# Kernel optimization log

Measured on AMD Instinct MI355X. Metric: run time of the kernel, lower is better.

The kernel has to match this reference:

```python
import jax, jax.numpy as jnp
import numpy as np

BN_EPS = 1e-5

def _bn(h, gamma, beta, mean, var):
    # inference-mode BatchNorm1d
    return (h - mean) * jax.lax.rsqrt(var + BN_EPS) * gamma + beta


def setup_inputs() -> dict:
    key = jax.random.key(0)
    ks = jax.random.split(key, 16)
    N, E, D_in, D, L = 100000, 640000, 256, 128, 3
    s = 0.05
    return {
        "x": jax.random.normal(ks[0], (N, D_in), jnp.float32),
        "edge_index": jax.random.randint(ks[1], (2, E), 0, N, jnp.int32),
        "W_in": jax.random.normal(ks[2], (D_in, D), jnp.float32) * s,
        "b_in": jax.random.normal(ks[3], (D,), jnp.float32) * s,
        "bn_in_gamma": jax.random.uniform(ks[4], (D,), jnp.float32, 0.5, 1.5),
        "bn_in_beta": jax.random.normal(ks[5], (D,), jnp.float32) * s,
        "bn_in_mean": jax.random.normal(ks[6], (D,), jnp.float32) * s,
        "bn_in_var": jax.random.uniform(ks[7], (D,), jnp.float32, 0.5, 1.5),
        "Wl": jax.random.normal(ks[8], (L, D, D), jnp.float32) * s,
        "bl": jax.random.normal(ks[9], (L, D), jnp.float32) * s,
        "Wr": jax.random.normal(ks[10], (L, D, D), jnp.float32) * s,
        "bn_gamma": jax.random.uniform(ks[11], (L, D), jnp.float32, 0.5, 1.5),
        "bn_beta": jax.random.normal(ks[12], (L, D), jnp.float32) * s,
        "bn_mean": jax.random.normal(ks[13], (L, D), jnp.float32) * s,
        "bn_var": jax.random.uniform(ks[14], (L, D), jnp.float32, 0.5, 1.5),
    }


def reference(x, edge_index, W_in, b_in, bn_in_gamma, bn_in_beta, bn_in_mean,
              bn_in_var, Wl, bl, Wr, bn_gamma, bn_beta, bn_mean, bn_var):
    N = x.shape[0]
    src, dst = edge_index[0], edge_index[1]
    # in-degree (clamped to 1 so isolated nodes aggregate to 0, matching PyG mean)
    deg = jax.ops.segment_sum(jnp.ones_like(dst, jnp.float32), dst, num_segments=N)
    deg = jnp.maximum(deg, 1.0)[:, None]  # [N, 1]

    # input projection + BN + ReLU (dropout = identity in eval)
    h = jax.nn.relu(_bn(x @ W_in + b_in, bn_in_gamma, bn_in_beta, bn_in_mean, bn_in_var))

    L = Wl.shape[0]
    for l in range(L):
        # SAGEConv(mean): lin_l(mean_j h_j) + lin_r(h_i)
        agg = jax.ops.segment_sum(h[src], dst, num_segments=N) / deg  # [N, D]
        h_new = agg @ Wl[l] + bl[l] + h @ Wr[l]
        h_new = jax.nn.relu(_bn(h_new, bn_gamma[l], bn_beta[l], bn_mean[l], bn_var[l]))
        h = h + h_new  # residual
    return h
```

## Files before the change

### kernel.cpp

```cpp
#include <hip/hip_runtime.h>

#define BN_EPS 1e-5f

typedef __bf16 bf16x8 __attribute__((ext_vector_type(8)));
typedef float f32x4 __attribute__((ext_vector_type(4)));
typedef unsigned int uint;
typedef unsigned short ushort;

__device__ __forceinline__ ushort f2bf(float f) {
  union { float f; uint u; } v; v.f = f;
  uint r = v.u + 0x7FFF + ((v.u >> 16) & 1);
  return (ushort)(r >> 16);
}
__device__ __forceinline__ float bf2f_lo(uint u) {
  union { uint i; float f; } v; v.i = u << 16; return v.f;
}
__device__ __forceinline__ float bf2f_hi(uint u) {
  union { uint i; float f; } v; v.i = u & 0xffff0000u; return v.f;
}
__device__ __forceinline__ uint pack2(float a, float b) {
  return (uint)f2bf(a) | ((uint)f2bf(b) << 16);
}

__device__ __forceinline__ void lds_barrier() {
  asm volatile("" ::: "memory");
  __builtin_amdgcn_s_waitcnt(0xC07F);
  __builtin_amdgcn_s_barrier();
  asm volatile("" ::: "memory");
}


__global__ void hist_kernel(const int* __restrict__ dst, int* __restrict__ cnt, int E) {
  int e = blockIdx.x * 256 + threadIdx.x;
  if (e < E) atomicAdd(&cnt[dst[e]], 1);
}

__device__ __forceinline__ int block_exscan256(int v, int tid, int* ws4) {
  __syncthreads();
  int lane = tid & 63, w = tid >> 6;
  int x = v;
  #pragma unroll
  for (int off = 1; off < 64; off <<= 1) {
    int y = __shfl_up(x, off, 64);
    if (lane >= off) x += y;
  }
  if (lane == 63) ws4[w] = x;
  __syncthreads();
  if (tid == 0) {
    int s = 0;
    for (int i = 0; i < 4; ++i) { int t = ws4[i]; ws4[i] = s; s += t; }
  }
  __syncthreads();
  return ws4[w] + x - v;
}

__global__ void blocksum_kernel(const int* __restrict__ cnt, int* __restrict__ bsum, int N) {
  __shared__ int ws4[4];
  int tid = threadIdx.x;
  int i = blockIdx.x * 256 + tid;
  int v = (i < N) ? cnt[i] : 0;
  #pragma unroll
  for (int off = 32; off > 0; off >>= 1) v += __shfl_down(v, off, 64);
  if ((tid & 63) == 0) ws4[tid >> 6] = v;
  __syncthreads();
  if (tid == 0) bsum[blockIdx.x] = ws4[0] + ws4[1] + ws4[2] + ws4[3];
}

__global__ void scanbsum_kernel(const int* __restrict__ bsum, int* __restrict__ boff,
                                int NB, int* __restrict__ rowptr, int N, int E) {
  __shared__ int ws4[4];
  __shared__ int tot;
  int tid = threadIdx.x;
  int carry = 0;
  for (int base = 0; base < NB; base += 256) {
    int i = base + tid;
    int v = (i < NB) ? bsum[i] : 0;
    int ex = block_exscan256(v, tid, ws4);
    if (i < NB) boff[i] = carry + ex;
    if (tid == 255) tot = ex + v;
    __syncthreads();
    carry += tot;
  }
  if (tid == 0) rowptr[N] = E;
}

__global__ void writerowptr_kernel(const int* __restrict__ cnt, const int* __restrict__ boff,
                                   int* __restrict__ rowptr, int N) {
  __shared__ int ws4[4];
  int tid = threadIdx.x;
  int i = blockIdx.x * 256 + tid;
  int v = (i < N) ? cnt[i] : 0;
  int ex = block_exscan256(v, tid, ws4);
  if (i < N) rowptr[i] = boff[blockIdx.x] + ex;
}

__global__ void fill_kernel(const int* __restrict__ src, const int* __restrict__ dst,
                            const int* __restrict__ rowptr, int* __restrict__ cur,
                            int* __restrict__ col, int E) {
  int e = blockIdx.x * 256 + threadIdx.x;
  if (e < E) {
    int d = dst[e];
    int p = rowptr[d] + atomicAdd(&cur[d], 1);
    col[p] = src[e];
  }
}

__global__ void deginv_kernel(const int* __restrict__ rowptr, float* __restrict__ dinv, int N) {
  int i = blockIdx.x * 256 + threadIdx.x;
  if (i < N) {
    int d = rowptr[i + 1] - rowptr[i];
    dinv[i] = 1.0f / (float)(d > 0 ? d : 1);
  }
}


__global__ void prep_weights_fm(const float* __restrict__ W_in, const float* __restrict__ Wl,
                                const float* __restrict__ Wr, ushort* __restrict__ Bfm) {
  int p = blockIdx.x * 256 + threadIdx.x;
  int mat = p >> 12;
  int rem = p & 4095;
  int half = rem >> 11;
  int rem2 = rem & 2047;
  int nt = rem2 >> 8, kt2 = (rem2 >> 6) & 3, lane = rem2 & 63;
  int n = nt * 16 + (lane & 15);
  int k0 = (half * 4 + kt2) * 32 + (lane >> 4) * 8;
  ushort tmp[8];
  #pragma unroll
  for (int j = 0; j < 8; ++j) {
    int k = k0 + j;
    float v;
    if (mat == 0) v = W_in[k * 128 + n];
    else {
      int l = mat - 1;
      v = (k < 128) ? Wl[l * 16384 + k * 128 + n] : Wr[l * 16384 + (k - 128) * 128 + n];
    }
    tmp[j] = f2bf(v);
  }
  *(uint4*)&Bfm[(size_t)p * 8] = *(const uint4*)tmp;
}


__global__ void agg_kernel(const int* __restrict__ rowptr, const int* __restrict__ col,
                           const float* __restrict__ dinv, const ushort* __restrict__ h,
                           ushort* __restrict__ agg, int N) {
  int node = blockIdx.x * 8 + (threadIdx.x >> 5);
  if (node >= N) return;
  int lane = threadIdx.x & 31;
  const ushort* hp = h + lane * 4;
  int beg = rowptr[node], end = rowptr[node + 1];
  float a0 = 0.f, a1 = 0.f, a2 = 0.f, a3 = 0.f;
  int e = beg;
  for (; e + 3 < end; e += 4) {
    uint2 v0 = *(const uint2*)(hp + (size_t)col[e] * 128);
    uint2 v1 = *(const uint2*)(hp + (size_t)col[e + 1] * 128);
    uint2 v2 = *(const uint2*)(hp + (size_t)col[e + 2] * 128);
    uint2 v3 = *(const uint2*)(hp + (size_t)col[e + 3] * 128);
    a0 += (bf2f_lo(v0.x) + bf2f_lo(v1.x)) + (bf2f_lo(v2.x) + bf2f_lo(v3.x));
    a1 += (bf2f_hi(v0.x) + bf2f_hi(v1.x)) + (bf2f_hi(v2.x) + bf2f_hi(v3.x));
    a2 += (bf2f_lo(v0.y) + bf2f_lo(v1.y)) + (bf2f_lo(v2.y) + bf2f_lo(v3.y));
    a3 += (bf2f_hi(v0.y) + bf2f_hi(v1.y)) + (bf2f_hi(v2.y) + bf2f_hi(v3.y));
  }
  for (; e < end; ++e) {
    uint2 v0 = *(const uint2*)(hp + (size_t)col[e] * 128);
    a0 += bf2f_lo(v0.x); a1 += bf2f_hi(v0.x);
    a2 += bf2f_lo(v0.y); a3 += bf2f_hi(v0.y);
  }
  float di = dinv[node];
  uint2 o;
  o.x = pack2(a0 * di, a1 * di);
  o.y = pack2(a2 * di, a3 * di);
  *(uint2*)(agg + (size_t)node * 128 + lane * 4) = o;
}


template<bool F32OUT>
__global__ __launch_bounds__(256, 3)
void gemm_layer(const ushort* __restrict__ A0, const ushort* __restrict__ A1,
                const ushort* __restrict__ Bfm, const float* __restrict__ bias,
                const float* __restrict__ gamma, const float* __restrict__ beta,
                const float* __restrict__ mean, const float* __restrict__ var,
                const ushort* __restrict__ residual, void* __restrict__ out, int N) {
  __shared__ ushort Bs[16384];
  int tid = threadIdx.x, wave = tid >> 6, lane = tid & 63;
  int wm = wave >> 1, wn = wave & 1, quad = lane >> 4, l16 = lane & 15;
  int m0 = blockIdx.x * 128;

  int rowm[4];
  #pragma unroll
  for (int mt = 0; mt < 4; ++mt) {
    int r = m0 + wm * 64 + mt * 16 + l16;
    rowm[mt] = r < N ? r : N - 1;
  }

  uint4 a_buf[2][4];
  #pragma unroll
  for (int mt = 0; mt < 4; ++mt)
    a_buf[0][mt] = *(const uint4*)(A0 + (size_t)rowm[mt] * 128 + quad * 8);

  #pragma unroll
  for (int i = 0; i < 8; ++i) {
    int idx = i * 256 + tid;
    *(uint4*)&Bs[idx * 8] = *(const uint4*)&Bfm[idx * 8];
  }
  lds_barrier();

  f32x4 acc[4][4] = {};

  #pragma unroll
  for (int h = 0; h < 2; ++h) {
    #pragma unroll
    for (int k2 = 0; k2 < 4; ++k2) {
      int kt = h * 4 + k2;
      if (kt < 7) {
        const ushort* bse = (kt + 1 < 4) ? A0 : A1;
        int ko = ((kt + 1) & 3) * 32 + quad * 8;
        #pragma unroll
        for (int mt = 0; mt < 4; ++mt)
          a_buf[(kt + 1) & 1][mt] = *(const uint4*)(bse + (size_t)rowm[mt] * 128 + ko);
      }
      bf16x8 bfr[4];
      #pragma unroll
      for (int nt = 0; nt < 4; ++nt)
        bfr[nt] = *(bf16x8*)&Bs[(((wn * 4 + nt) * 4 + k2) * 64 + lane) * 8];
      #pragma unroll
      for (int mt = 0; mt < 4; ++mt) {
        bf16x8 af = __builtin_bit_cast(bf16x8, a_buf[kt & 1][mt]);
        #pragma unroll
        for (int nt = 0; nt < 4; ++nt)
          acc[mt][nt] = __builtin_amdgcn_mfma_f32_16x16x32_bf16(af, bfr[nt], acc[mt][nt], 0, 0, 0);
      }
    }
    if (h == 0) {
      lds_barrier();
      #pragma unroll
      for (int i = 0; i < 8; ++i) {
        int idx = i * 256 + tid;
        *(uint4*)&Bs[idx * 8] = *(const uint4*)&Bfm[16384 + idx * 8];
      }
      lds_barrier();
    }
  }

  #pragma unroll
  for (int nt = 0; nt < 4; ++nt) {
    int c = wn * 64 + nt * 16 + l16;
    float sc = gamma[c] * rsqrtf(var[c] + BN_EPS);
    float sh = beta[c] - mean[c] * sc;
    float bi = bias[c];
    #pragma unroll
    for (int mt = 0; mt < 4; ++mt)
      #pragma unroll
      for (int r = 0; r < 4; ++r)
        acc[mt][nt][r] = fmaxf((acc[mt][nt][r] + bi) * sc + sh, 0.f);
  }

  lds_barrier();
  float* Cb = (float*)Bs + wave * (16 * 68);
  #pragma unroll
  for (int mt = 0; mt < 4; ++mt) {
    #pragma unroll
    for (int nt = 0; nt < 4; ++nt)
      #pragma unroll
      for (int r = 0; r < 4; ++r)
        Cb[(quad * 4 + r) * 68 + nt * 16 + l16] = acc[mt][nt][r];
    #pragma unroll
    for (int i = 0; i < 4; ++i) {
      int idx = i * 64 + lane, rowl = idx >> 4, seg = idx & 15;
      int grow = m0 + wm * 64 + mt * 16 + rowl;
      if (grow < N) {
        float4 vv = *(float4*)&Cb[rowl * 68 + seg * 4];
        uint2 rv = *(const uint2*)(residual + (size_t)grow * 128 + wn * 64 + seg * 4);
        vv.x += bf2f_lo(rv.x); vv.y += bf2f_hi(rv.x);
        vv.z += bf2f_lo(rv.y); vv.w += bf2f_hi(rv.y);
        if (F32OUT) {
          *(float4*)((float*)out + (size_t)grow * 128 + wn * 64 + seg * 4) = vv;
        } else {
          uint2 o;
          o.x = pack2(vv.x, vv.y); o.y = pack2(vv.z, vv.w);
          *(uint2*)((ushort*)out + (size_t)grow * 128 + wn * 64 + seg * 4) = o;
        }
      }
    }
  }
}


__global__ __launch_bounds__(256, 3)
void gemm_in(const float* __restrict__ X, const ushort* __restrict__ Bfm,
             const float* __restrict__ bias,
             const float* __restrict__ gamma, const float* __restrict__ beta,
             const float* __restrict__ mean, const float* __restrict__ var,
             ushort* __restrict__ out, int N) {
  __shared__ ushort Bs[16384];
  int tid = threadIdx.x, wave = tid >> 6, lane = tid & 63;
  int wm = wave >> 1, wn = wave & 1, quad = lane >> 4, l16 = lane & 15;
  int m0 = blockIdx.x * 128;

  int rowm[4];
  #pragma unroll
  for (int mt = 0; mt < 4; ++mt) {
    int r = m0 + wm * 64 + mt * 16 + l16;
    rowm[mt] = r < N ? r : N - 1;
  }

  float4 f_buf[2][4][2];
  #pragma unroll
  for (int mt = 0; mt < 4; ++mt) {
    const float* p = X + (size_t)rowm[mt] * 256 + quad * 8;
    f_buf[0][mt][0] = *(const float4*)p;
    f_buf[0][mt][1] = *(const float4*)(p + 4);
  }

  #pragma unroll
  for (int i = 0; i < 8; ++i) {
    int idx = i * 256 + tid;
    *(uint4*)&Bs[idx * 8] = *(const uint4*)&Bfm[idx * 8];
  }
  lds_barrier();

  f32x4 acc[4][4] = {};

  #pragma unroll
  for (int h = 0; h < 2; ++h) {
    #pragma unroll
    for (int k2 = 0; k2 < 4; ++k2) {
      int kt = h * 4 + k2;
      if (kt < 7) {
        int ko = (kt + 1) * 32 + quad * 8;
        #pragma unroll
        for (int mt = 0; mt < 4; ++mt) {
          const float* p = X + (size_t)rowm[mt] * 256 + ko;
          f_buf[(kt + 1) & 1][mt][0] = *(const float4*)p;
          f_buf[(kt + 1) & 1][mt][1] = *(const float4*)(p + 4);
        }
      }
      bf16x8 bfr[4];
      #pragma unroll
      for (int nt = 0; nt < 4; ++nt)
        bfr[nt] = *(bf16x8*)&Bs[(((wn * 4 + nt) * 4 + k2) * 64 + lane) * 8];
      #pragma unroll
      for (int mt = 0; mt < 4; ++mt) {
        float4 lo = f_buf[kt & 1][mt][0], hi = f_buf[kt & 1][mt][1];
        uint4 av;
        av.x = pack2(lo.x, lo.y); av.y = pack2(lo.z, lo.w);
        av.z = pack2(hi.x, hi.y); av.w = pack2(hi.z, hi.w);
        bf16x8 af = __builtin_bit_cast(bf16x8, av);
        #pragma unroll
        for (int nt = 0; nt < 4; ++nt)
          acc[mt][nt] = __builtin_amdgcn_mfma_f32_16x16x32_bf16(af, bfr[nt], acc[mt][nt], 0, 0, 0);
      }
    }
    if (h == 0) {
      lds_barrier();
      #pragma unroll
      for (int i = 0; i < 8; ++i) {
        int idx = i * 256 + tid;
        *(uint4*)&Bs[idx * 8] = *(const uint4*)&Bfm[16384 + idx * 8];
      }
      lds_barrier();
    }
  }

  #pragma unroll
  for (int nt = 0; nt < 4; ++nt) {
    int c = wn * 64 + nt * 16 + l16;
    float sc = gamma[c] * rsqrtf(var[c] + BN_EPS);
    float sh = beta[c] - mean[c] * sc;
    float bi = bias[c];
    #pragma unroll
    for (int mt = 0; mt < 4; ++mt)
      #pragma unroll
      for (int r = 0; r < 4; ++r)
        acc[mt][nt][r] = fmaxf((acc[mt][nt][r] + bi) * sc + sh, 0.f);
  }

  lds_barrier();
  float* Cb = (float*)Bs + wave * (16 * 68);
  #pragma unroll
  for (int mt = 0; mt < 4; ++mt) {
    #pragma unroll
    for (int nt = 0; nt < 4; ++nt)
      #pragma unroll
      for (int r = 0; r < 4; ++r)
        Cb[(quad * 4 + r) * 68 + nt * 16 + l16] = acc[mt][nt][r];
    #pragma unroll
    for (int i = 0; i < 4; ++i) {
      int idx = i * 64 + lane, rowl = idx >> 4, seg = idx & 15;
      int grow = m0 + wm * 64 + mt * 16 + rowl;
      if (grow < N) {
        float4 vv = *(float4*)&Cb[rowl * 68 + seg * 4];
        uint2 o;
        o.x = pack2(vv.x, vv.y); o.y = pack2(vv.z, vv.w);
        *(uint2*)(out + (size_t)grow * 128 + wn * 64 + seg * 4) = o;
      }
    }
  }
}


extern "C" void kernel_launch(void* const* d_in, const int* in_sizes, int n_in,
                              void* d_out, int out_size, void* d_ws, size_t ws_size,
                              hipStream_t stream) {
  const float* x      = (const float*)d_in[0];
  const int*   eidx   = (const int*)d_in[1];
  const float* W_in   = (const float*)d_in[2];
  const float* b_in   = (const float*)d_in[3];
  const float* bng_in = (const float*)d_in[4];
  const float* bnb_in = (const float*)d_in[5];
  const float* bnm_in = (const float*)d_in[6];
  const float* bnv_in = (const float*)d_in[7];
  const float* Wl     = (const float*)d_in[8];
  const float* bl     = (const float*)d_in[9];
  const float* Wr     = (const float*)d_in[10];
  const float* bng    = (const float*)d_in[11];
  const float* bnb    = (const float*)d_in[12];
  const float* bnm    = (const float*)d_in[13];
  const float* bnv    = (const float*)d_in[14];

  const int N = in_sizes[0] / 256;
  const int E = in_sizes[1] / 2;
  const int NB = (N + 255) / 256;
  const int* src = eidx;
  const int* dst = eidx + E;

  char* ws = (char*)d_ws;
  size_t off = 0;
  auto alloc = [&](size_t bytes) {
    void* p = ws + off;
    off = (off + bytes + 255) & ~(size_t)255;
    return p;
  };
  int* cnt      = (int*)alloc((size_t)N * 4);
  int* rowptr   = (int*)alloc((size_t)(N + 1) * 4);
  int* bsum     = (int*)alloc((size_t)NB * 4);
  int* boff     = (int*)alloc((size_t)NB * 4);
  int* col      = (int*)alloc((size_t)E * 4);
  float* dinv   = (float*)alloc((size_t)N * 4);
  ushort* Bfm   = (ushort*)alloc(4 * 32768 * 2);
  ushort* hA    = (ushort*)alloc((size_t)N * 128 * 2);
  ushort* hB    = (ushort*)alloc((size_t)N * 128 * 2);
  ushort* agg   = (ushort*)alloc((size_t)N * 128 * 2);
  (void)ws_size; (void)n_in; (void)out_size;

  const int EB = (E + 255) / 256;
  const int GB = (N + 127) / 128;

  hipMemsetAsync(cnt, 0, (size_t)N * 4, stream);
  hist_kernel<<<EB, 256, 0, stream>>>(dst, cnt, E);
  blocksum_kernel<<<NB, 256, 0, stream>>>(cnt, bsum, N);
  scanbsum_kernel<<<1, 256, 0, stream>>>(bsum, boff, NB, rowptr, N, E);
  writerowptr_kernel<<<NB, 256, 0, stream>>>(cnt, boff, rowptr, N);
  hipMemsetAsync(cnt, 0, (size_t)N * 4, stream);
  fill_kernel<<<EB, 256, 0, stream>>>(src, dst, rowptr, cnt, col, E);
  deginv_kernel<<<NB, 256, 0, stream>>>(rowptr, dinv, N);

  prep_weights_fm<<<64, 256, 0, stream>>>(W_in, Wl, Wr, Bfm);

  gemm_in<<<GB, 256, 0, stream>>>(x, Bfm, b_in, bng_in, bnb_in, bnm_in, bnv_in, hA, N);

  ushort* hbuf[2] = { hA, hB };
  for (int l = 0; l < 3; ++l) {
    const ushort* h_in = hbuf[l & 1];
    agg_kernel<<<(N + 7) / 8, 256, 0, stream>>>(rowptr, col, dinv, h_in, agg, N);
    const ushort* BfmL = Bfm + (size_t)(l + 1) * 32768;
    const float* biasL = bl + l * 128;
    if (l < 2) {
      gemm_layer<false><<<GB, 256, 0, stream>>>(agg, h_in, BfmL, biasL,
          bng + l * 128, bnb + l * 128, bnm + l * 128, bnv + l * 128,
          h_in, (void*)hbuf[(l + 1) & 1], N);
    } else {
      gemm_layer<true><<<GB, 256, 0, stream>>>(agg, h_in, BfmL, biasL,
          bng + l * 128, bnb + l * 128, bnm + l * 128, bnv + l * 128,
          h_in, d_out, N);
    }
  }
}
```

Before: 490.8 us.

## Load GEMM weight fragments directly from global into registers instead of LDS

The GEMM kernels no longer stage the 32 KB weight panel into LDS with barriers. Each wave now double-buffers its B fragments straight from global memory (which should hit in L2/cache) alongside the A prefetch, and LDS is shrunk to just the epilogue staging buffer. This removes the barrier stalls and the large LDS footprint, which can raise occupancy, at the cost of more global load traffic and register pressure. The gemm_in occupancy hint drops from 3 to 2 blocks per SM. Separately, the degree-inverse kernel is removed and 1/deg is computed inline in the aggregation kernel.

```diff
diff --git a/kernel.cpp b/kernel.cpp
--- a/kernel.cpp
+++ b/kernel.cpp
@@ -20,13 +20,6 @@
 }
 __device__ __forceinline__ uint pack2(float a, float b) {
   return (uint)f2bf(a) | ((uint)f2bf(b) << 16);
-}
-
-__device__ __forceinline__ void lds_barrier() {
-  asm volatile("" ::: "memory");
-  __builtin_amdgcn_s_waitcnt(0xC07F);
-  __builtin_amdgcn_s_barrier();
-  asm volatile("" ::: "memory");
 }
 
 
@@ -105,14 +98,6 @@
   }
 }
 
-__global__ void deginv_kernel(const int* __restrict__ rowptr, float* __restrict__ dinv, int N) {
-  int i = blockIdx.x * 256 + threadIdx.x;
-  if (i < N) {
-    int d = rowptr[i + 1] - rowptr[i];
-    dinv[i] = 1.0f / (float)(d > 0 ? d : 1);
-  }
-}
-
 
 __global__ void prep_weights_fm(const float* __restrict__ W_in, const float* __restrict__ Wl,
                                 const float* __restrict__ Wr, ushort* __restrict__ Bfm) {
@@ -141,13 +126,14 @@
 
 
 __global__ void agg_kernel(const int* __restrict__ rowptr, const int* __restrict__ col,
-                           const float* __restrict__ dinv, const ushort* __restrict__ h,
-                           ushort* __restrict__ agg, int N) {
+                           const ushort* __restrict__ h, ushort* __restrict__ agg, int N) {
   int node = blockIdx.x * 8 + (threadIdx.x >> 5);
   if (node >= N) return;
   int lane = threadIdx.x & 31;
   const ushort* hp = h + lane * 4;
   int beg = rowptr[node], end = rowptr[node + 1];
+  int deg = end - beg;
+  float di = 1.0f / (float)(deg > 0 ? deg : 1);
   float a0 = 0.f, a1 = 0.f, a2 = 0.f, a3 = 0.f;
   int e = beg;
   for (; e + 3 < end; e += 4) {
@@ -165,7 +151,6 @@
     a0 += bf2f_lo(v0.x); a1 += bf2f_hi(v0.x);
     a2 += bf2f_lo(v0.y); a3 += bf2f_hi(v0.y);
   }
-  float di = dinv[node];
   uint2 o;
   o.x = pack2(a0 * di, a1 * di);
   o.y = pack2(a2 * di, a3 * di);
@@ -180,7 +165,7 @@
                 const float* __restrict__ gamma, const float* __restrict__ beta,
                 const float* __restrict__ mean, const float* __restrict__ var,
                 const ushort* __restrict__ residual, void* __restrict__ out, int N) {
-  __shared__ ushort Bs[16384];
+  __shared__ float Cb_all[4 * 16 * 68];
   int tid = threadIdx.x, wave = tid >> 6, lane = tid & 63;
   int wm = wave >> 1, wn = wave & 1, quad = lane >> 4, l16 = lane & 15;
   int m0 = blockIdx.x * 128;
@@ -192,52 +177,42 @@
     rowm[mt] = r < N ? r : N - 1;
   }
 
-  uint4 a_buf[2][4];
+  uint4 a_buf[2][4], b_buf[2][4];
   #pragma unroll
   for (int mt = 0; mt < 4; ++mt)
     a_buf[0][mt] = *(const uint4*)(A0 + (size_t)rowm[mt] * 128 + quad * 8);
-
-  #pragma unroll
-  for (int i = 0; i < 8; ++i) {
-    int idx = i * 256 + tid;
-    *(uint4*)&Bs[idx * 8] = *(const uint4*)&Bfm[idx * 8];
-  }
-  lds_barrier();
+  {
+    const ushort* bp = Bfm + (size_t)(wn * 4 * 256 + lane) * 8;
+    #pragma unroll
+    for (int nt = 0; nt < 4; ++nt)
+      b_buf[0][nt] = *(const uint4*)(bp + nt * 2048);
+  }
 
   f32x4 acc[4][4] = {};
 
   #pragma unroll
-  for (int h = 0; h < 2; ++h) {
-    #pragma unroll
-    for (int k2 = 0; k2 < 4; ++k2) {
-      int kt = h * 4 + k2;
-      if (kt < 7) {
-        const ushort* bse = (kt + 1 < 4) ? A0 : A1;
-        int ko = ((kt + 1) & 3) * 32 + quad * 8;
-        #pragma unroll
-        for (int mt = 0; mt < 4; ++mt)
-          a_buf[(kt + 1) & 1][mt] = *(const uint4*)(bse + (size_t)rowm[mt] * 128 + ko);
-      }
-      bf16x8 bfr[4];
+  for (int kt = 0; kt < 8; ++kt) {
+    if (kt < 7) {
+      int k1 = kt + 1;
+      const ushort* bse = (k1 < 4) ? A0 : A1;
+      int ko = (k1 & 3) * 32 + quad * 8;
+      #pragma unroll
+      for (int mt = 0; mt < 4; ++mt)
+        a_buf[k1 & 1][mt] = *(const uint4*)(bse + (size_t)rowm[mt] * 128 + ko);
+      const ushort* bp = Bfm + ((size_t)(k1 >> 2) * 16384 +
+                                (size_t)((wn * 4) * 256 + (k1 & 3) * 64 + lane) * 8);
       #pragma unroll
       for (int nt = 0; nt < 4; ++nt)
-        bfr[nt] = *(bf16x8*)&Bs[(((wn * 4 + nt) * 4 + k2) * 64 + lane) * 8];
-      #pragma unroll
-      for (int mt = 0; mt < 4; ++mt) {
-        bf16x8 af = __builtin_bit_cast(bf16x8, a_buf[kt & 1][mt]);
-        #pragma unroll
-        for (int nt = 0; nt < 4; ++nt)
-          acc[mt][nt] = __builtin_amdgcn_mfma_f32_16x16x32_bf16(af, bfr[nt], acc[mt][nt], 0, 0, 0);
-      }
-    }
-    if (h == 0) {
-      lds_barrier();
-      #pragma unroll
-      for (int i = 0; i < 8; ++i) {
-        int idx = i * 256 + tid;
-        *(uint4*)&Bs[idx * 8] = *(const uint4*)&Bfm[16384 + idx * 8];
-      }
-      lds_barrier();
+        b_buf[k1 & 1][nt] = *(const uint4*)(bp + nt * 2048);
+    }
+    __builtin_amdgcn_sched_barrier(0);
+    #pragma unroll
+    for (int mt = 0; mt < 4; ++mt) {
+      bf16x8 af = __builtin_bit_cast(bf16x8, a_buf[kt & 1][mt]);
+      #pragma unroll
+      for (int nt = 0; nt < 4; ++nt)
+        acc[mt][nt] = __builtin_amdgcn_mfma_f32_16x16x32_bf16(
+            af, __builtin_bit_cast(bf16x8, b_buf[kt & 1][nt]), acc[mt][nt], 0, 0, 0);
     }
   }
 
@@ -254,8 +229,7 @@
         acc[mt][nt][r] = fmaxf((acc[mt][nt][r] + bi) * sc + sh, 0.f);
   }
 
-  lds_barrier();
-  float* Cb = (float*)Bs + wave * (16 * 68);
+  float* Cb = Cb_all + wave * (16 * 68);
   #pragma unroll
   for (int mt = 0; mt < 4; ++mt) {
     #pragma unroll
@@ -285,13 +259,13 @@
 }
 
 
-__global__ __launch_bounds__(256, 3)
+__global__ __launch_bounds__(256, 2)
 void gemm_in(const float* __restrict__ X, const ushort* __restrict__ Bfm,
              const float* __restrict__ bias,
              const float* __restrict__ gamma, const float* __restrict__ beta,
              const float* __restrict__ mean, const float* __restrict__ var,
              ushort* __restrict__ out, int N) {
-  __shared__ ushort Bs[16384];
+  __shared__ float Cb_all[4 * 16 * 68];
   int tid = threadIdx.x, wave = tid >> 6, lane = tid & 63;
   int wm = wave >> 1, wn = wave & 1, quad = lane >> 4, l16 = lane & 15;
   int m0 = blockIdx.x * 128;
@@ -304,60 +278,51 @@
   }
 
   float4 f_buf[2][4][2];
+  uint4 b_buf[2][4];
   #pragma unroll
   for (int mt = 0; mt < 4; ++mt) {
     const float* p = X + (size_t)rowm[mt] * 256 + quad * 8;
     f_buf[0][mt][0] = *(const float4*)p;
     f_buf[0][mt][1] = *(const float4*)(p + 4);
   }
-
-  #pragma unroll
-  for (int i = 0; i < 8; ++i) {
-    int idx = i * 256 + tid;
-    *(uint4*)&Bs[idx * 8] = *(const uint4*)&Bfm[idx * 8];
-  }
-  lds_barrier();
+  {
+    const ushort* bp = Bfm + (size_t)(wn * 4 * 256 + lane) * 8;
+    #pragma unroll
+    for (int nt = 0; nt < 4; ++nt)
+      b_buf[0][nt] = *(const uint4*)(bp + nt * 2048);
+  }
 
   f32x4 acc[4][4] = {};
 
   #pragma unroll
-  for (int h = 0; h < 2; ++h) {
-    #pragma unroll
-    for (int k2 = 0; k2 < 4; ++k2) {
-      int kt = h * 4 + k2;
-      if (kt < 7) {
-        int ko = (kt + 1) * 32 + quad * 8;
-        #pragma unroll
-        for (int mt = 0; mt < 4; ++mt) {
-          const float* p = X + (size_t)rowm[mt] * 256 + ko;
-          f_buf[(kt + 1) & 1][mt][0] = *(const float4*)p;
-          f_buf[(kt + 1) & 1][mt][1] = *(const float4*)(p + 4);
-        }
+  for (int kt = 0; kt < 8; ++kt) {
+    if (kt < 7) {
+      int k1 = kt + 1;
+      int ko = k1 * 32 + quad * 8;
+      #pragma unroll
+      for (int mt = 0; mt < 4; ++mt) {
+        const float* p = X + (size_t)rowm[mt] * 256 + ko;
+        f_buf[k1 & 1][mt][0] = *(const float4*)p;
+        f_buf[k1 & 1][mt][1] = *(const float4*)(p + 4);
       }
-      bf16x8 bfr[4];
+      const ushort* bp = Bfm + ((size_t)(k1 >> 2) * 16384 +
+                                (size_t)((wn * 4) * 256 + (k1 & 3) * 64 + lane) * 8);
       #pragma unroll
       for (int nt = 0; nt < 4; ++nt)
-        bfr[nt] = *(bf16x8*)&Bs[(((wn * 4 + nt) * 4 + k2) * 64 + lane) * 8];
-      #pragma unroll
-      for (int mt = 0; mt < 4; ++mt) {
-        float4 lo = f_buf[kt & 1][mt][0], hi = f_buf[kt & 1][mt][1];
-        uint4 av;
-        av.x = pack2(lo.x, lo.y); av.y = pack2(lo.z, lo.w);
-        av.z = pack2(hi.x, hi.y); av.w = pack2(hi.z, hi.w);
-        bf16x8 af = __builtin_bit_cast(bf16x8, av);
-        #pragma unroll
-        for (int nt = 0; nt < 4; ++nt)
-          acc[mt][nt] = __builtin_amdgcn_mfma_f32_16x16x32_bf16(af, bfr[nt], acc[mt][nt], 0, 0, 0);
-      }
-    }
-    if (h == 0) {
-      lds_barrier();
-      #pragma unroll
-      for (int i = 0; i < 8; ++i) {
-        int idx = i * 256 + tid;
-        *(uint4*)&Bs[idx * 8] = *(const uint4*)&Bfm[16384 + idx * 8];
-      }
-      lds_barrier();
+        b_buf[k1 & 1][nt] = *(const uint4*)(bp + nt * 2048);
+    }
+    __builtin_amdgcn_sched_barrier(0);
+    #pragma unroll
+    for (int mt = 0; mt < 4; ++mt) {
+      float4 lo = f_buf[kt & 1][mt][0], hi = f_buf[kt & 1][mt][1];
+      uint4 av;
+      av.x = pack2(lo.x, lo.y); av.y = pack2(lo.z, lo.w);
+      av.z = pack2(hi.x, hi.y); av.w = pack2(hi.z, hi.w);
+      bf16x8 af = __builtin_bit_cast(bf16x8, av);
+      #pragma unroll
+      for (int nt = 0; nt < 4; ++nt)
+        acc[mt][nt] = __builtin_amdgcn_mfma_f32_16x16x32_bf16(
+            af, __builtin_bit_cast(bf16x8, b_buf[kt & 1][nt]), acc[mt][nt], 0, 0, 0);
     }
   }
 
@@ -374,8 +339,7 @@
         acc[mt][nt][r] = fmaxf((acc[mt][nt][r] + bi) * sc + sh, 0.f);
   }
 
-  lds_barrier();
-  float* Cb = (float*)Bs + wave * (16 * 68);
+  float* Cb = Cb_all + wave * (16 * 68);
   #pragma unroll
   for (int mt = 0; mt < 4; ++mt) {
     #pragma unroll
@@ -435,7 +399,6 @@
   int* bsum     = (int*)alloc((size_t)NB * 4);
   int* boff     = (int*)alloc((size_t)NB * 4);
   int* col      = (int*)alloc((size_t)E * 4);
-  float* dinv   = (float*)alloc((size_t)N * 4);
   ushort* Bfm   = (ushort*)alloc(4 * 32768 * 2);
   ushort* hA    = (ushort*)alloc((size_t)N * 128 * 2);
   ushort* hB    = (ushort*)alloc((size_t)N * 128 * 2);
@@ -452,7 +415,6 @@
   writerowptr_kernel<<<NB, 256, 0, stream>>>(cnt, boff, rowptr, N);
   hipMemsetAsync(cnt, 0, (size_t)N * 4, stream);
   fill_kernel<<<EB, 256, 0, stream>>>(src, dst, rowptr, cnt, col, E);
-  deginv_kernel<<<NB, 256, 0, stream>>>(rowptr, dinv, N);
 
   prep_weights_fm<<<64, 256, 0, stream>>>(W_in, Wl, Wr, Bfm);
 
@@ -461,7 +423,7 @@
   ushort* hbuf[2] = { hA, hB };
   for (int l = 0; l < 3; ++l) {
     const ushort* h_in = hbuf[l & 1];
-    agg_kernel<<<(N + 7) / 8, 256, 0, stream>>>(rowptr, col, dinv, h_in, agg, N);
+    agg_kernel<<<(N + 7) / 8, 256, 0, stream>>>(rowptr, col, h_in, agg, N);
     const ushort* BfmL = Bfm + (size_t)(l + 1) * 32768;
     const float* biasL = bl + l * 128;
     if (l < 2) {
```

Measured after the change: 479.1 us. -2.4%, faster.
